# Kernel optimization log

Measured on AMD Instinct MI355X. Metric: run time of the kernel, lower is better.

## Reference

```python
import jax, jax.numpy as jnp
import numpy as np

N_NODES = 100000
N_EDGES = 1000000
D = 128
NEG_SLOPE = 0.01  # F.leaky_relu default


def setup_inputs() -> dict:
    key = jax.random.key(0)
    k1, k2, k3, k4, k5, k6 = jax.random.split(key, 6)
    h_src = jax.random.normal(k1, (N_NODES, D), dtype=jnp.float32)
    h_dst = jax.random.normal(k2, (N_NODES, D), dtype=jnp.float32)
    edge_src = jax.random.randint(k3, (N_EDGES,), 0, N_NODES, dtype=jnp.int32)
    edge_dst = jax.random.randint(k4, (N_EDGES,), 0, N_NODES, dtype=jnp.int32)
    # xavier_normal_ on a (1, D) tensor -> std = sqrt(2/(1+D))
    std = float(np.sqrt(2.0 / (1.0 + D)))
    attn_l = jax.random.normal(k5, (D,), dtype=jnp.float32) * std
    attn_r = jax.random.normal(k6, (D,), dtype=jnp.float32) * std
    bias = jnp.zeros((D,), dtype=jnp.float32)
    return {"h_src": h_src, "h_dst": h_dst, "edge_src": edge_src,
            "edge_dst": edge_dst, "attn_l": attn_l, "attn_r": attn_r,
            "bias": bias}


def reference(h_src, h_dst, edge_src, edge_dst, attn_l, attn_r, bias):
    # Per-node attention projections (dot with attn vectors): [N]
    el = h_src @ attn_l
    er = h_dst @ attn_r
    # Edge scores: gather + add + leaky_relu, [E]
    e = jax.nn.leaky_relu(el[edge_src] + er[edge_dst], negative_slope=NEG_SLOPE)
    # Segment (per-destination) softmax over incoming edges
    m = jax.ops.segment_max(e, edge_dst, num_segments=N_NODES)  # [N]
    a = jnp.exp(e - m[edge_dst])                                # [E]
    s = jax.ops.segment_sum(a, edge_dst, num_segments=N_NODES)  # [N]
    alpha = a / s[edge_dst]                                     # [E]
    # dropout p=0.0 -> identity
    # Weighted message + scatter-sum aggregation: [N, D]
    msg = h_src[edge_src] * alpha[:, None]                      # [E, D]
    h_N = jax.ops.segment_sum(msg, edge_dst, num_segments=N_NODES)
    return h_N + bias
```

## Files before the change

### kernel.cpp

```cpp
#include <hip/hip_runtime.h>
#include <math.h>

#define N_NODES 100000
#define N_EDGES 1000000
#define D 128
#define NEG_SLOPE 0.01f
#define SCAN_BLOCK 1024
#define N_SCAN_BLOCKS ((N_NODES + SCAN_BLOCK - 1) / SCAN_BLOCK)

__device__ __forceinline__ unsigned int f2bf(float f) {
    unsigned int u = __float_as_uint(f);
    return (u + 0x7FFFu + ((u >> 16) & 1u)) >> 16;
}

__global__ void node_proj_cvt_kernel(const float* __restrict__ h_src,
                                     const float* __restrict__ h_dst,
                                     const float* __restrict__ attn_l,
                                     const float* __restrict__ attn_r,
                                     float* __restrict__ el,
                                     float* __restrict__ er,
                                     unsigned int* __restrict__ hbf) {
    int node = (blockIdx.x * blockDim.x + threadIdx.x) >> 6;
    int lane = threadIdx.x & 63;
    if (node >= N_NODES) return;
    float2 vs = ((const float2*)(h_src + (size_t)node * D))[lane];
    float2 vd = ((const float2*)(h_dst + (size_t)node * D))[lane];
    float2 wl = ((const float2*)attn_l)[lane];
    float2 wr = ((const float2*)attn_r)[lane];
    hbf[(size_t)node * 64 + lane] = f2bf(vs.x) | (f2bf(vs.y) << 16);
    float sl = vs.x * wl.x + vs.y * wl.y;
    float sr = vd.x * wr.x + vd.y * wr.y;
    #pragma unroll
    for (int off = 32; off > 0; off >>= 1) {
        sl += __shfl_down(sl, off, 64);
        sr += __shfl_down(sr, off, 64);
    }
    if (lane == 0) { el[node] = sl; er[node] = sr; }
}

__global__ void edge_w_slot_kernel(const int* __restrict__ esrc,
                                   const int* __restrict__ edst,
                                   const float* __restrict__ el,
                                   const float* __restrict__ er,
                                   float* __restrict__ w,
                                   int* __restrict__ slot,
                                   int* __restrict__ cnt) {
    int i = blockIdx.x * blockDim.x + threadIdx.x;
    if (i >= N_EDGES) return;
    int s = esrc[i], d = edst[i];
    float v = el[s] + er[d];
    v = (v > 0.0f) ? v : NEG_SLOPE * v;
    w[i] = __expf(v);
    slot[i] = atomicAdd(&cnt[d], 1);
}

__global__ void scan1_kernel(const int* __restrict__ cnt,
                             int* __restrict__ row_start,
                             int* __restrict__ blocksum) {
    __shared__ int buf[2][SCAN_BLOCK];
    int tid = threadIdx.x;
    int gid = blockIdx.x * SCAN_BLOCK + tid;
    int x = (gid < N_NODES) ? cnt[gid] : 0;
    int pi = 0;
    buf[0][tid] = x;
    __syncthreads();
    for (int off = 1; off < SCAN_BLOCK; off <<= 1) {
        int v = buf[pi][tid];
        if (tid >= off) v += buf[pi][tid - off];
        buf[1 - pi][tid] = v;
        pi = 1 - pi;
        __syncthreads();
    }
    int incl = buf[pi][tid];
    if (gid < N_NODES) row_start[gid + 1] = incl;
    if (tid == SCAN_BLOCK - 1) blocksum[blockIdx.x] = incl;
    if (gid == 0) row_start[0] = 0;
}

__global__ void scan2_kernel(int* __restrict__ blocksum) {
    __shared__ int buf[2][128];
    int tid = threadIdx.x;
    int x = (tid < N_SCAN_BLOCKS) ? blocksum[tid] : 0;
    int pi = 0;
    buf[0][tid] = x;
    __syncthreads();
    for (int off = 1; off < 128; off <<= 1) {
        int v = buf[pi][tid];
        if (tid >= off) v += buf[pi][tid - off];
        buf[1 - pi][tid] = v;
        pi = 1 - pi;
        __syncthreads();
    }
    int incl = buf[pi][tid];
    if (tid < N_SCAN_BLOCKS) blocksum[tid] = incl - x;
}

__global__ void scan3_kernel(int* __restrict__ row_start,
                             const int* __restrict__ blocksum) {
    int gid = blockIdx.x * SCAN_BLOCK + threadIdx.x;
    if (gid < N_NODES) row_start[gid + 1] += blocksum[blockIdx.x];
}

__global__ void fill_kernel(const int* __restrict__ esrc,
                            const int* __restrict__ edst,
                            const int* __restrict__ slot,
                            const float* __restrict__ w,
                            const int* __restrict__ row_start,
                            int2* __restrict__ csr) {
    int i = blockIdx.x * blockDim.x + threadIdx.x;
    if (i >= N_EDGES) return;
    int d = edst[i];
    int2 p;
    p.x = esrc[i];
    p.y = __float_as_int(w[i]);
    csr[row_start[d] + slot[i]] = p;
}

__global__ void aggregate_kernel(const unsigned int* __restrict__ hbf,
                                 const int* __restrict__ row_start,
                                 const int2* __restrict__ csr,
                                 const float* __restrict__ bias,
                                 float* __restrict__ out) {
    int node = (blockIdx.x * blockDim.x + threadIdx.x) >> 6;
    int lane = threadIdx.x & 63;
    if (node >= N_NODES) return;
    int start = row_start[node];
    int deg = row_start[node + 1] - start;
    float2 b2 = ((const float2*)bias)[lane];
    float2* op = (float2*)(out + (size_t)node * D) + lane;
    if (deg == 0) { *op = b2; return; }

    float sum = 0.0f, accx = 0.0f, accy = 0.0f;
    for (int base = 0; base < deg; base += 64) {
        int j = base + lane;
        float wv = 0.0f;
        int sv = 0;
        if (j < deg) {
            int2 p = csr[start + j];
            sv = p.x;
            wv = __int_as_float(p.y);
        }
        int nrem = min(64, deg - base);
        for (int k = 0; k < nrem; ++k) {
            float wk = __shfl(wv, k, 64);
            int   sk = __shfl(sv, k, 64);
            unsigned int g = hbf[(size_t)sk * 64 + lane];
            accx += wk * __uint_as_float(g << 16);
            accy += wk * __uint_as_float(g & 0xFFFF0000u);
        }
        float ws = wv;
        #pragma unroll
        for (int off = 32; off > 0; off >>= 1) ws += __shfl_xor(ws, off, 64);
        sum += ws;
    }

    float inv = 1.0f / sum;
    float2 o = { accx * inv + b2.x, accy * inv + b2.y };
    *op = o;
}

extern "C" void kernel_launch(void* const* d_in, const int* in_sizes, int n_in,
                              void* d_out, int out_size, void* d_ws, size_t ws_size,
                              hipStream_t stream) {
    const float* h_src  = (const float*)d_in[0];
    const float* h_dst  = (const float*)d_in[1];
    const int*   esrc   = (const int*)d_in[2];
    const int*   edst   = (const int*)d_in[3];
    const float* attn_l = (const float*)d_in[4];
    const float* attn_r = (const float*)d_in[5];
    const float* bias   = (const float*)d_in[6];
    float* out = (float*)d_out;

    int2*         csr       = (int2*)d_ws;
    unsigned int* hbf       = (unsigned int*)(csr + N_EDGES);
    float*        el        = (float*)(hbf + (size_t)N_NODES*64);
    float*        er        = el + N_NODES;
    int*          cnt       = (int*)(er + N_NODES);
    int*          row_start = cnt + N_NODES;
    int*          blocksum  = row_start + N_NODES + 1;
    float*        w         = (float*)(blocksum + 128);
    int*          slot      = (int*)(w + N_EDGES);

    hipMemsetAsync(cnt, 0, N_NODES * sizeof(int), stream);

    node_proj_cvt_kernel<<<(N_NODES + 3) / 4, 256, 0, stream>>>(
        h_src, h_dst, attn_l, attn_r, el, er, hbf);

    edge_w_slot_kernel<<<(N_EDGES + 255) / 256, 256, 0, stream>>>(
        esrc, edst, el, er, w, slot, cnt);

    scan1_kernel<<<N_SCAN_BLOCKS, SCAN_BLOCK, 0, stream>>>(cnt, row_start, blocksum);
    scan2_kernel<<<1, 128, 0, stream>>>(blocksum);
    scan3_kernel<<<N_SCAN_BLOCKS, SCAN_BLOCK, 0, stream>>>(row_start, blocksum);

    fill_kernel<<<(N_EDGES + 255) / 256, 256, 0, stream>>>(
        esrc, edst, slot, w, row_start, csr);

    aggregate_kernel<<<(N_NODES + 3) / 4, 256, 0, stream>>>(
        hbf, row_start, csr, bias, out);
}
```

Before: 293.5 us.

## Fuse scan into single-pass decoupled lookback and split edges across quarter-waves

The three-kernel prefix scan becomes one kernel that uses a decoupled lookback over per-block status flags, and the cnt memset is folded into the projection kernel. The aggregation kernel now processes four edges per iteration, one per 16-lane quarter-wave, with each lane loading 16 bytes of bf16 features, then reduces the partial sums across quarters with shuffles. This is meant to cut launch count and increase memory-level parallelism in the gather. The lookback spins on flags from earlier blocks, so it depends on blocks making forward progress, and the final cross-quarter reduction adds shuffle work.

```diff
diff --git a/kernel.cpp b/kernel.cpp
--- a/kernel.cpp
+++ b/kernel.cpp
@@ -19,8 +19,13 @@
                                      const float* __restrict__ attn_r,
                                      float* __restrict__ el,
                                      float* __restrict__ er,
-                                     unsigned int* __restrict__ hbf) {
-    int node = (blockIdx.x * blockDim.x + threadIdx.x) >> 6;
+                                     unsigned int* __restrict__ hbf,
+                                     int* __restrict__ cnt,
+                                     unsigned long long* __restrict__ st) {
+    int t = blockIdx.x * blockDim.x + threadIdx.x;
+    if (t < N_NODES) cnt[t] = 0;
+    if (t < N_SCAN_BLOCKS) st[t] = 0ULL;
+    int node = t >> 6;
     int lane = threadIdx.x & 63;
     if (node >= N_NODES) return;
     float2 vs = ((const float2*)(h_src + (size_t)node * D))[lane];
@@ -54,10 +59,11 @@
     slot[i] = atomicAdd(&cnt[d], 1);
 }
 
-__global__ void scan1_kernel(const int* __restrict__ cnt,
-                             int* __restrict__ row_start,
-                             int* __restrict__ blocksum) {
+__global__ void scan_kernel(const int* __restrict__ cnt,
+                            int* __restrict__ row_start,
+                            unsigned long long* __restrict__ st) {
     __shared__ int buf[2][SCAN_BLOCK];
+    __shared__ int s_running;
     int tid = threadIdx.x;
     int gid = blockIdx.x * SCAN_BLOCK + tid;
     int x = (gid < N_NODES) ? cnt[gid] : 0;
@@ -72,33 +78,37 @@
         __syncthreads();
     }
     int incl = buf[pi][tid];
-    if (gid < N_NODES) row_start[gid + 1] = incl;
-    if (tid == SCAN_BLOCK - 1) blocksum[blockIdx.x] = incl;
+    int total = buf[pi][SCAN_BLOCK - 1];
+    if (tid == 0) {
+        if (blockIdx.x == 0) {
+            __hip_atomic_store(&st[0], (2ULL << 32) | (unsigned int)total,
+                               __ATOMIC_RELEASE, __HIP_MEMORY_SCOPE_AGENT);
+            s_running = 0;
+        } else {
+            __hip_atomic_store(&st[blockIdx.x], (1ULL << 32) | (unsigned int)total,
+                               __ATOMIC_RELEASE, __HIP_MEMORY_SCOPE_AGENT);
+            int running = 0;
+            int j = blockIdx.x - 1;
+            for (;;) {
+                unsigned long long s;
+                do {
+                    s = __hip_atomic_load(&st[j], __ATOMIC_ACQUIRE,
+                                          __HIP_MEMORY_SCOPE_AGENT);
+                } while ((s >> 32) == 0);
+                running += (int)(unsigned int)s;
+                if ((s >> 32) == 2) break;
+                --j;
+            }
+            __hip_atomic_store(&st[blockIdx.x],
+                               (2ULL << 32) | (unsigned int)(running + total),
+                               __ATOMIC_RELEASE, __HIP_MEMORY_SCOPE_AGENT);
+            s_running = running;
+        }
+    }
+    __syncthreads();
+    int running = s_running;
+    if (gid < N_NODES) row_start[gid + 1] = running + incl;
     if (gid == 0) row_start[0] = 0;
-}
-
-__global__ void scan2_kernel(int* __restrict__ blocksum) {
-    __shared__ int buf[2][128];
-    int tid = threadIdx.x;
-    int x = (tid < N_SCAN_BLOCKS) ? blocksum[tid] : 0;
-    int pi = 0;
-    buf[0][tid] = x;
-    __syncthreads();
-    for (int off = 1; off < 128; off <<= 1) {
-        int v = buf[pi][tid];
-        if (tid >= off) v += buf[pi][tid - off];
-        buf[1 - pi][tid] = v;
-        pi = 1 - pi;
-        __syncthreads();
-    }
-    int incl = buf[pi][tid];
-    if (tid < N_SCAN_BLOCKS) blocksum[tid] = incl - x;
-}
-
-__global__ void scan3_kernel(int* __restrict__ row_start,
-                             const int* __restrict__ blocksum) {
-    int gid = blockIdx.x * SCAN_BLOCK + threadIdx.x;
-    if (gid < N_NODES) row_start[gid + 1] += blocksum[blockIdx.x];
 }
 
 __global__ void fill_kernel(const int* __restrict__ esrc,
@@ -121,42 +131,52 @@
                                  const int2* __restrict__ csr,
                                  const float* __restrict__ bias,
                                  float* __restrict__ out) {
-    int node = (blockIdx.x * blockDim.x + threadIdx.x) >> 6;
+    int t = blockIdx.x * blockDim.x + threadIdx.x;
+    int node = t >> 6;
+    if (node >= N_NODES) return;
     int lane = threadIdx.x & 63;
-    if (node >= N_NODES) return;
+    int q = lane >> 4, ql = lane & 15;
     int start = row_start[node];
     int deg = row_start[node + 1] - start;
-    float2 b2 = ((const float2*)bias)[lane];
-    float2* op = (float2*)(out + (size_t)node * D) + lane;
-    if (deg == 0) { *op = b2; return; }
-
-    float sum = 0.0f, accx = 0.0f, accy = 0.0f;
-    for (int base = 0; base < deg; base += 64) {
-        int j = base + lane;
-        float wv = 0.0f;
-        int sv = 0;
-        if (j < deg) {
-            int2 p = csr[start + j];
-            sv = p.x;
-            wv = __int_as_float(p.y);
-        }
-        int nrem = min(64, deg - base);
-        for (int k = 0; k < nrem; ++k) {
-            float wk = __shfl(wv, k, 64);
-            int   sk = __shfl(sv, k, 64);
-            unsigned int g = hbf[(size_t)sk * 64 + lane];
-            accx += wk * __uint_as_float(g << 16);
-            accy += wk * __uint_as_float(g & 0xFFFF0000u);
-        }
-        float ws = wv;
+    float4 b0 = ((const float4*)bias)[ql * 2];
+    float4 b1 = ((const float4*)bias)[ql * 2 + 1];
+    float4* op = (float4*)(out + (size_t)node * D);
+    if (deg == 0) {
+        if (q == 0) { op[ql * 2] = b0; op[ql * 2 + 1] = b1; }
+        return;
+    }
+    float acc[8] = {0, 0, 0, 0, 0, 0, 0, 0};
+    float sum = 0.0f;
+    for (int base = 0; base < deg; base += 4) {
+        int e = base + q;
+        int2 p = csr[start + min(e, deg - 1)];
+        float wk = (e < deg) ? __int_as_float(p.y) : 0.0f;
+        uint4 g = ((const uint4*)(hbf + (size_t)p.x * 64))[ql];
+        acc[0] += wk * __uint_as_float(g.x << 16);
+        acc[1] += wk * __uint_as_float(g.x & 0xFFFF0000u);
+        acc[2] += wk * __uint_as_float(g.y << 16);
+        acc[3] += wk * __uint_as_float(g.y & 0xFFFF0000u);
+        acc[4] += wk * __uint_as_float(g.z << 16);
+        acc[5] += wk * __uint_as_float(g.z & 0xFFFF0000u);
+        acc[6] += wk * __uint_as_float(g.w << 16);
+        acc[7] += wk * __uint_as_float(g.w & 0xFFFF0000u);
+        sum += wk;
+    }
+    #pragma unroll
+    for (int off = 16; off <= 32; off <<= 1) {
+        sum += __shfl_xor(sum, off, 64);
         #pragma unroll
-        for (int off = 32; off > 0; off >>= 1) ws += __shfl_xor(ws, off, 64);
-        sum += ws;
-    }
-
-    float inv = 1.0f / sum;
-    float2 o = { accx * inv + b2.x, accy * inv + b2.y };
-    *op = o;
+        for (int i = 0; i < 8; ++i) acc[i] += __shfl_xor(acc[i], off, 64);
+    }
+    if (q == 0) {
+        float inv = 1.0f / sum;
+        float4 o0 = { acc[0] * inv + b0.x, acc[1] * inv + b0.y,
+                      acc[2] * inv + b0.z, acc[3] * inv + b0.w };
+        float4 o1 = { acc[4] * inv + b1.x, acc[5] * inv + b1.y,
+                      acc[6] * inv + b1.z, acc[7] * inv + b1.w };
+        op[ql * 2]     = o0;
+        op[ql * 2 + 1] = o1;
+    }
 }
 
 extern "C" void kernel_launch(void* const* d_in, const int* in_sizes, int n_in,
@@ -171,27 +191,23 @@
     const float* bias   = (const float*)d_in[6];
     float* out = (float*)d_out;
 
-    int2*         csr       = (int2*)d_ws;
-    unsigned int* hbf       = (unsigned int*)(csr + N_EDGES);
-    float*        el        = (float*)(hbf + (size_t)N_NODES*64);
-    float*        er        = el + N_NODES;
-    int*          cnt       = (int*)(er + N_NODES);
-    int*          row_start = cnt + N_NODES;
-    int*          blocksum  = row_start + N_NODES + 1;
-    float*        w         = (float*)(blocksum + 128);
-    int*          slot      = (int*)(w + N_EDGES);
-
-    hipMemsetAsync(cnt, 0, N_NODES * sizeof(int), stream);
+    int2*               csr       = (int2*)d_ws;
+    unsigned int*       hbf       = (unsigned int*)(csr + N_EDGES);
+    unsigned long long* st        = (unsigned long long*)(hbf + (size_t)N_NODES * 64);
+    float*              el        = (float*)(st + 128);
+    float*              er        = el + N_NODES;
+    int*                cnt       = (int*)(er + N_NODES);
+    int*                row_start = cnt + N_NODES;
+    float*              w         = (float*)(row_start + N_NODES + 2);
+    int*                slot      = (int*)(w + N_EDGES);
 
     node_proj_cvt_kernel<<<(N_NODES + 3) / 4, 256, 0, stream>>>(
-        h_src, h_dst, attn_l, attn_r, el, er, hbf);
+        h_src, h_dst, attn_l, attn_r, el, er, hbf, cnt, st);
 
     edge_w_slot_kernel<<<(N_EDGES + 255) / 256, 256, 0, stream>>>(
         esrc, edst, el, er, w, slot, cnt);
 
-    scan1_kernel<<<N_SCAN_BLOCKS, SCAN_BLOCK, 0, stream>>>(cnt, row_start, blocksum);
-    scan2_kernel<<<1, 128, 0, stream>>>(blocksum);
-    scan3_kernel<<<N_SCAN_BLOCKS, SCAN_BLOCK, 0, stream>>>(row_start, blocksum);
+    scan_kernel<<<N_SCAN_BLOCKS, SCAN_BLOCK, 0, stream>>>(cnt, row_start, st);
 
     fill_kernel<<<(N_EDGES + 255) / 256, 256, 0, stream>>>(
         esrc, edst, slot, w, row_start, csr);
```

Result: faster. 276.1 us (-5.9%).
